# Kernel tuning notes

Measured on AMD Instinct MI355X. Metric: run time of the kernel, lower is better.

## Reference

```python
import jax, jax.numpy as jnp
import numpy as np
from itertools import combinations

A = 4          # anchor_points
K = 16         # neighbor_num
INTRA = A * (A - 1) // 2   # 6
CH = INTRA * 2 + A * A     # 28 = generator channels
B, N, S = 1, 8192, 4096
CIN, COUT = 64, 128


def cdist(x):
    # pairwise euclidean distances [B,N,N], zero-safe sqrt (zero grad at d=0)
    sq = jnp.sum(x * x, -1)
    d2 = sq[:, :, None] + sq[:, None, :] - 2.0 * jnp.einsum('bnc,bmc->bnm', x, x)
    d2 = jnp.maximum(d2, 0.0)
    m = d2 > 0
    return jnp.where(m, jnp.sqrt(jnp.where(m, d2, 1.0)), 0.0)


def index_points(points, idx):
    # points [B,N,...], idx [B,*] -> [B,*,...]
    return jax.vmap(lambda p, i: p[i])(points, idx)


def index_points_dists(dists, i1, i2):
    # dists [B,N,N]; result[b,...] = dists[b, i1[b,...], i2[b,...]]
    i1, i2 = jnp.broadcast_arrays(i1, i2)
    return jax.vmap(lambda d, a, b: d[a, b])(dists, i1, i2)


def generator(xyz):
    # RotationInvariantDistFea.forward(xyz, concat_raw_relative_fea=True)
    D = cdist(xyz)
    neg_nd, ni = jax.lax.top_k(-D, K)   # K >= A; smallest-K, sorted ascending
    nd = -neg_nd
    ai = ni[:, :, :A]
    # intra-anchor dists: dists to anchors 1..A-1 plus pairwise dists among them
    subs = [index_points_dists(D, ai[:, :, pi], ai[:, :, pj])[:, :, None]
            for pi, pj in combinations(range(1, A), 2)]
    intra = jnp.concatenate([nd[:, :, 1:A]] + subs, axis=2)  # [B,P,6]
    # inter-anchor dists: center anchors x neighbor anchors -> [B,P,K,A*A]
    nai = index_points(ai, ni)                                # [B,P,K,A]
    inter = index_points_dists(D, ai[:, :, None, :, None],
                               nai[:, :, :, None, :]).reshape(D.shape[0], D.shape[1], K, A * A)
    center = jnp.broadcast_to(intra[:, :, None, :], (intra.shape[0], intra.shape[1], K, INTRA))
    rf = jnp.concatenate([center, index_points(intra, ni), inter], axis=3)  # [B,P,K,28]
    return rf, ni, D


def mlp(x, W, b, g, be, act):
    # Linear + BatchNorm1d (training mode: stats over batch*points) + optional leaky_relu(0.2)
    y = x @ W + b
    mu = jnp.mean(y, (0, 1))
    var = jnp.var(y, (0, 1))
    y = (y - mu) * jax.lax.rsqrt(var + 1e-5) * g + be
    return jax.nn.leaky_relu(y, 0.2) if act else y


def forward(xyz, feature, sample_indexes, Ww, bw, gw, betaw, Wb, bb, gb, betab, Wo, bo, go, betao):
    rf_before, ni_before, D_before = generator(xyz)
    intra_before = rf_before[:, :, 0, :INTRA]
    xyz_s = index_points(xyz, sample_indexes)
    feat = index_points(feature, sample_indexes)
    intra_before = index_points(intra_before, sample_indexes)
    rf_after, ni_after, _ = generator(xyz_s)
    intra_after = rf_after[:, :, 0, :INTRA]
    a_before = index_points(ni_before[:, :, :A], sample_indexes)                  # [B,S,A]
    a_after = jax.vmap(lambda s, a: s[a])(sample_indexes, ni_after[:, :, :A])     # map to global idx
    inter = index_points_dists(D_before, a_before[:, :, :, None],
                               a_after[:, :, None, :]).reshape(B, S, A * A)
    adf = jnp.concatenate([intra_before, intra_after, inter], axis=2)             # [B,S,28]
    w = mlp(adf, Ww, bw, gw, betaw, False)
    bia = mlp(adf, Wb, bb, gb, betab, False)
    feat = jax.nn.leaky_relu(feat * w + bia, 0.2)
    feat = jnp.concatenate([feat, adf], axis=2)                                   # [B,S,92]
    feat = mlp(feat, Wo, bo, go, betao, True)                                     # [B,S,128]
    return xyz_s, feat, rf_after, ni_after


def setup_inputs():
    key = jax.random.key(0)
    ks = jax.random.split(key, 8)
    xyz = jax.random.normal(ks[0], (B, N, 3), jnp.float32)
    feature = jax.random.normal(ks[1], (B, N, CIN), jnp.float32)
    sample_indexes = jnp.stack([jax.random.permutation(jax.random.fold_in(ks[2], i), N)[:S]
                                for i in range(B)]).astype(jnp.int32)

    def lin(k, cin, cout):
        k1, k2 = jax.random.split(k)
        W = jax.random.normal(k1, (cin, cout), jnp.float32) / np.float32(np.sqrt(cin))
        b = jax.random.normal(k2, (cout,), jnp.float32) * 0.01
        return W, b, jnp.ones((cout,), jnp.float32), jnp.zeros((cout,), jnp.float32)

    Ww, bw, gw, betaw = lin(ks[5], CH, CIN)
    Wb, bb, gb, betab = lin(ks[6], CH, CIN)
    Wo, bo, go, betao = lin(ks[7], CH + CIN, COUT)
    return dict(xyz=xyz, feature=feature, sample_indexes=sample_indexes,
                Ww=Ww, bw=bw, gw=gw, betaw=betaw,
                Wb=Wb, bb=bb, gb=gb, betab=betab,
                Wo=Wo, bo=bo, go=go, betao=betao)


def reference(xyz, feature, sample_indexes, Ww, bw, gw, betaw, Wb, bb, gb, betab, Wo, bo, go, betao):
    return forward(xyz, feature, sample_indexes, Ww, bw, gw, betaw, Wb, bb, gb, betab, Wo, bo, go, betao)
```

## Files before the change

### kernel.cpp

```cpp
#include <hip/hip_runtime.h>
#include <hip/hip_bf16.h>
#include <math.h>

#define N_PTS 8192
#define S_PTS 4096
typedef unsigned long long u64;
typedef unsigned u32;

__device__ __forceinline__ float pair_dist_d(const float4 a, const float4 b) {
    double ax = a.x, ay = a.y, az = a.z;
    double bx = b.x, by = b.y, bz = b.z;
    double dx = ax - bx, dy = ay - by, dz = az - bz;
    double d2 = dx * dx + dy * dy + dz * dz;
    return d2 > 0.0 ? (float)sqrt(d2) : 0.0f;
}

__device__ __forceinline__ float d2_f32_gram(const float4 a, const float4 b) {
    float dot = __fadd_rn(__fadd_rn(__fmul_rn(a.x, b.x), __fmul_rn(a.y, b.y)),
                          __fmul_rn(a.z, b.z));
    float d2 = __fsub_rn(__fadd_rn(a.w, b.w), __fmul_rn(2.0f, dot));
    return fmaxf(d2, 0.0f);
}

__global__ __launch_bounds__(256) void stage_kernel(
        const float* __restrict__ xyz, const int* __restrict__ sidx,
        float4* __restrict__ cb, float4* __restrict__ ca,
        float* __restrict__ out_xyz_s) {
    int i = blockIdx.x * blockDim.x + threadIdx.x;
    if (i < N_PTS) {
        float x = xyz[i * 3 + 0], y = xyz[i * 3 + 1], z = xyz[i * 3 + 2];
        float sq = __fadd_rn(__fadd_rn(__fmul_rn(x, x), __fmul_rn(y, y)),
                             __fmul_rn(z, z));
        cb[i] = make_float4(x, y, z, sq);
    }
    if (i < S_PTS) {
        int si = sidx[i];
        float x = xyz[si * 3 + 0], y = xyz[si * 3 + 1], z = xyz[si * 3 + 2];
        float sq = __fadd_rn(__fadd_rn(__fmul_rn(x, x), __fmul_rn(y, y)),
                             __fmul_rn(z, z));
        ca[i] = make_float4(x, y, z, sq);
        out_xyz_s[i * 3 + 0] = x;
        out_xyz_s[i * 3 + 1] = y;
        out_xyz_s[i * 3 + 2] = z;
    }
}


template <int KOUT, int ITERS>
__device__ u64 knn_full_ladder(const float4 q, const float4* __restrict__ cand,
                               int lane) {
    u32 Lk[KOUT], Li[KOUT];
#pragma unroll
    for (int j = 0; j < KOUT; ++j) { Lk[j] = 0xFFFFFFFFu; Li[j] = 0xFFFFFFFFu; }
    int c = lane;
    for (int tt = 0; tt < ITERS; ++tt, c += 64) {
        float d2 = d2_f32_gram(q, cand[c]);
        float Df = d2 > 0.0f ? __fsqrt_rn(d2) : 0.0f;
        u32 kb = __float_as_uint(Df);
        if (kb < Lk[KOUT - 1]) {
#pragma unroll
            for (int j = KOUT - 1; j >= 1; --j) {
                bool up = kb < Lk[j - 1], ins = kb < Lk[j];
                Lk[j] = up ? Lk[j - 1] : (ins ? kb : Lk[j]);
                Li[j] = up ? Li[j - 1] : (ins ? (u32)c : Li[j]);
            }
            bool i0 = kb < Lk[0];
            Lk[0] = i0 ? kb : Lk[0];
            Li[0] = i0 ? (u32)c : Li[0];
        }
    }
    u64 Lu[KOUT];
#pragma unroll
    for (int j = 0; j < KOUT; ++j) Lu[j] = ((u64)Lk[j] << 32) | (u64)Li[j];
    u64 res = ~0ull;
#pragma unroll
    for (int r = 0; r < KOUT; ++r) {
        u64 m = Lu[0];
#pragma unroll
        for (int off = 32; off >= 1; off >>= 1) {
            u64 o = __shfl_xor(m, off, 64);
            m = (o < m) ? o : m;
        }
        if (lane == r) res = m;
        if (Lu[0] == m) {
#pragma unroll
            for (int j = 0; j < KOUT - 1; ++j) Lu[j] = Lu[j + 1];
            Lu[KOUT - 1] = ~0ull;
        }
    }
    return res;
}

template <int J, int K, int NC>
__device__ u64 knn_select(const float4 q, const float4* __restrict__ cand,
                          int t, u32* mins, u64* buf, u32* shm) {
    int lane = t & 63, wid = t >> 6;
    u32 d2b[J];
    u32 m = 0xFFFFFFFFu;
#pragma unroll
    for (int j = 0; j < J; ++j) {
        float d2 = d2_f32_gram(q, cand[t + 256 * j]);
        u32 b = __float_as_uint(d2);
        d2b[j] = b;
        m = b < m ? b : m;
    }
    mins[t] = m;
    __syncthreads();
    if (wid == 0) {
        u32 v = mins[lane];
        u32 v2 = mins[lane + 64];  v = v2 < v ? v2 : v;
        v2 = mins[lane + 128];     v = v2 < v ? v2 : v;
        v2 = mins[lane + 192];     v = v2 < v ? v2 : v;
#pragma unroll
        for (int k = 2; k <= 64; k <<= 1) {
#pragma unroll
            for (int j2 = k >> 1; j2 >= 1; j2 >>= 1) {
                u32 o = __shfl_xor(v, j2, 64);
                bool keepMin = (((lane & j2) == 0) == ((lane & k) == 0));
                bool less = o < v;
                v = keepMin ? (less ? o : v) : (less ? v : o);
            }
        }
        if (lane == K - 1) shm[0] = v;
    }
    __syncthreads();
    u32 tau = shm[0];
    u32 c = 0;
#pragma unroll
    for (int j = 0; j < J; ++j) c += (d2b[j] <= tau) ? 1u : 0u;
    u32 x = c;
#pragma unroll
    for (int off = 1; off < 64; off <<= 1) {
        u32 y = __shfl_up(x, off, 64);
        if (lane >= off) x += y;
    }
    if (lane == 63) shm[1 + wid] = x;
    __syncthreads();
    u32 base = x - c;
    for (int w = 0; w < wid; ++w) base += shm[1 + w];
    u32 cnt = shm[1] + shm[2] + shm[3] + shm[4];
    if (cnt <= 256u) {
        u32 off = base;
#pragma unroll
        for (int j = 0; j < J; ++j) {
            if (d2b[j] <= tau) {
                float d2 = __uint_as_float(d2b[j]);
                float D = d2 > 0.0f ? __fsqrt_rn(d2) : 0.0f;
                buf[off++] = ((u64)__float_as_uint(D) << 32) |
                             (u64)(u32)(t + 256 * j);
            }
        }
    }
    __syncthreads();
    u64 res = ~0ull;
    if (wid == 0) {
        if (cnt <= 64u) {
            u64 v = (lane < (int)cnt) ? buf[lane] : ~0ull;
#pragma unroll
            for (int k = 2; k <= 64; k <<= 1) {
#pragma unroll
                for (int j2 = k >> 1; j2 >= 1; j2 >>= 1) {
                    u64 o = __shfl_xor(v, j2, 64);
                    bool keepMin = (((lane & j2) == 0) == ((lane & k) == 0));
                    bool less = o < v;
                    v = keepMin ? (less ? o : v) : (less ? v : o);
                }
            }
            res = v;
        } else if (cnt <= 256u) {
            u64 L0 = ~0ull, L1 = ~0ull, L2 = ~0ull, L3 = ~0ull;
            for (u32 mm = lane; mm < cnt; mm += 64) {
                u64 kk = buf[mm];
                if (kk < L3) {
                    if (kk < L1) {
                        L3 = L2; L2 = L1;
                        if (kk < L0) { L1 = L0; L0 = kk; } else L1 = kk;
                    } else {
                        if (kk < L2) { L3 = L2; L2 = kk; } else L3 = kk;
                    }
                }
            }
#pragma unroll
            for (int r = 0; r < K; ++r) {
                u64 mr = L0;
#pragma unroll
                for (int off = 32; off >= 1; off >>= 1) {
                    u64 o = __shfl_xor(mr, off, 64);
                    mr = (o < mr) ? o : mr;
                }
                if (lane == r) res = mr;
                if (L0 == mr) { L0 = L1; L1 = L2; L2 = L3; L3 = ~0ull; }
            }
        } else {
            res = knn_full_ladder<K, NC / 64>(q, cand, lane);
        }
    }
    return res;
}

__global__ __launch_bounds__(256, 4) void knn_kernel(
        const float4* __restrict__ cb, const float4* __restrict__ ca,
        const int* __restrict__ sidx,
        int* __restrict__ a_before, float* __restrict__ intra_before,
        int* __restrict__ ni_i, float* __restrict__ intra_after,
        float* __restrict__ out_ni) {
    __shared__ u32 mins[256];
    __shared__ u64 buf[256];
    __shared__ u32 shm[8];
    int t = threadIdx.x, lane = t & 63, wid = t >> 6;
    int bid = blockIdx.x;
    if (bid < S_PTS) {
        int s = bid;
        float4 q = ca[s];
        u64 res = knn_select<16, 16, 4096>(q, ca, t, mins, buf, shm);
        if (wid == 0) {
            int idx = (int)(res & 0xffffffffull);
            if (lane < 16) {
                ni_i[s * 16 + lane] = idx;
                out_ni[s * 16 + lane] = (float)idx;
            }
            if (lane >= 1 && lane < 4)
                intra_after[s * 6 + (lane - 1)] = pair_dist_d(q, ca[idx]);
            int i1 = __shfl(idx, 1, 64);
            int i2 = __shfl(idx, 2, 64);
            int i3 = __shfl(idx, 3, 64);
            if (lane < 3) {
                int pa = (lane == 2) ? i2 : i1;
                int pb = (lane == 0) ? i2 : i3;
                intra_after[s * 6 + 3 + lane] = pair_dist_d(ca[pa], ca[pb]);
            }
        }
    } else {
        int s = bid - S_PTS;
        float4 q = cb[sidx[s]];
        u64 res = knn_select<32, 4, 8192>(q, cb, t, mins, buf, shm);
        if (wid == 0) {
            int idx = (int)(res & 0xffffffffull);
            if (lane < 4) a_before[s * 4 + lane] = idx;
            if (lane >= 1 && lane < 4)
                intra_before[s * 6 + (lane - 1)] = pair_dist_d(q, cb[idx]);
            int i1 = __shfl(idx, 1, 64);
            int i2 = __shfl(idx, 2, 64);
            int i3 = __shfl(idx, 3, 64);
            if (lane < 3) {
                int pa = (lane == 2) ? i2 : i1;
                int pb = (lane == 0) ? i2 : i3;
                intra_before[s * 6 + 3 + lane] = pair_dist_d(cb[pa], cb[pb]);
            }
        }
    }
}

__global__ __launch_bounds__(256) void assemble_kernel(
        const float4* __restrict__ ca, const float4* __restrict__ cb,
        const int* __restrict__ ni_i, const float* __restrict__ intra_after,
        const int* __restrict__ a_before, const float* __restrict__ intra_before,
        const int* __restrict__ sidx,
        float* __restrict__ out_rf, float* __restrict__ adf) {
    __shared__ int s_ni[4][16];
    __shared__ float s_rf[4][16 * 28];
    __shared__ float s_ia[4][8];
    int t = threadIdx.x, wid = t >> 6, lane = t & 63;
    int s = blockIdx.x * 4 + wid;
    if (lane < 16) s_ni[wid][lane] = ni_i[s * 16 + lane];
    if (lane < 6) s_ia[wid][lane] = intra_after[s * 6 + lane];
    __syncthreads();

    int k = lane >> 2, qq = lane & 3;
    int nai_q = ni_i[s_ni[wid][k] * 16 + qq];
    float4 pq = ca[nai_q];
#pragma unroll
    for (int p = 0; p < 4; ++p) {
        float4 pp = ca[s_ni[wid][p]];
        s_rf[wid][k * 28 + 12 + p * 4 + qq] = pair_dist_d(pp, pq);
    }
    for (int idx = lane; idx < 16 * 12; idx += 64) {
        int kk = idx / 12, c = idx % 12;
        float v = (c < 6) ? s_ia[wid][c] : intra_after[s_ni[wid][kk] * 6 + (c - 6)];
        s_rf[wid][kk * 28 + c] = v;
    }
    if (lane < 16) {
        int p = lane >> 2, q2 = lane & 3;
        int ib = a_before[s * 4 + p];
        int ia = sidx[s_ni[wid][q2]];
        adf[s * 28 + 12 + lane] = pair_dist_d(cb[ib], cb[ia]);
    } else if (lane >= 32 && lane < 38) {
        adf[s * 28 + (lane - 32)] = intra_before[s * 6 + (lane - 32)];
    } else if (lane >= 40 && lane < 46) {
        adf[s * 28 + 6 + (lane - 40)] = s_ia[wid][lane - 40];
    }
    __syncthreads();
    const int base = s * 16 * 28;
    for (int idx = lane; idx < 16 * 28; idx += 64) out_rf[base + idx] = s_rf[wid][idx];
}

__global__ __launch_bounds__(256) void mlp1_kernel(
        const float* __restrict__ adf,
        const float* __restrict__ Ww, const float* __restrict__ bw,
        const float* __restrict__ Wb, const float* __restrict__ bb,
        float* __restrict__ y_wb) {
    __shared__ float sW[28 * 128];
    __shared__ float sb[128];
    __shared__ float sA[32 * 28];
    int t = threadIdx.x;
    for (int i = t; i < 28 * 128; i += 256) {
        int k = i >> 7, c = i & 127;
        sW[i] = (c < 64) ? Ww[k * 64 + c] : Wb[k * 64 + (c - 64)];
    }
    if (t < 128) sb[t] = (t < 64) ? bw[t] : bb[t - 64];
    int s0 = blockIdx.x * 32;
    for (int i = t; i < 32 * 28; i += 256) sA[i] = adf[s0 * 28 + i];
    __syncthreads();
    int sl = t >> 3, grp = t & 7;
    int s = s0 + sl;
    float acc[16];
#pragma unroll
    for (int k = 0; k < 16; ++k) acc[k] = sb[grp * 16 + k];
    for (int k2 = 0; k2 < 28; ++k2) {
        float a = sA[sl * 28 + k2];
#pragma unroll
        for (int k = 0; k < 16; ++k)
            acc[k] = fmaf(a, sW[k2 * 128 + grp * 16 + k], acc[k]);
    }
#pragma unroll
    for (int k = 0; k < 16; ++k) y_wb[(grp * 16 + k) * 4096 + s] = acc[k];
}

__global__ __launch_bounds__(256) void stats_kernel(
        const float* __restrict__ y,
        const float* __restrict__ g0, const float* __restrict__ be0,
        const float* __restrict__ g1, const float* __restrict__ be1, int csplit,
        float* __restrict__ scale, float* __restrict__ shift) {
    int c = blockIdx.x;
    const float* p = y + c * 4096;
    float s1 = 0.0f, s2 = 0.0f;
    for (int i = threadIdx.x; i < 4096; i += 256) {
        float v = p[i];
        s1 += v;
        s2 = fmaf(v, v, s2);
    }
    __shared__ float l1[256], l2[256];
    l1[threadIdx.x] = s1;
    l2[threadIdx.x] = s2;
    __syncthreads();
    for (int off = 128; off; off >>= 1) {
        if (threadIdx.x < off) {
            l1[threadIdx.x] += l1[threadIdx.x + off];
            l2[threadIdx.x] += l2[threadIdx.x + off];
        }
        __syncthreads();
    }
    if (threadIdx.x == 0) {
        float mean = l1[0] * (1.0f / 4096.0f);
        float var = l2[0] * (1.0f / 4096.0f) - mean * mean;
        float g = (c < csplit) ? g0[c] : g1[c - csplit];
        float be = (c < csplit) ? be0[c] : be1[c - csplit];
        float sc = g / sqrtf(var + 1e-5f);
        scale[c] = sc;
        shift[c] = be - mean * sc;
    }
}

__global__ __launch_bounds__(256) void mlp2_kernel(
        const float* __restrict__ y_wb,
        const float* __restrict__ scale1, const float* __restrict__ shift1,
        const float* __restrict__ feature, const int* __restrict__ sidx,
        const float* __restrict__ adf,
        const float* __restrict__ Wo, const float* __restrict__ bo,
        float* __restrict__ y_o) {
    __shared__ float sW[92 * 128];
    __shared__ float t2[16 * 129];
    __shared__ float scat[16 * 92];
    int t = threadIdx.x;
    int s0 = blockIdx.x * 16;
    for (int i = t; i < 92 * 128; i += 256) sW[i] = Wo[i];
    for (int i = t; i < 16 * 128; i += 256) {
        int row = i & 15, c = i >> 4;
        t2[row * 129 + c] = fmaf(y_wb[c * 4096 + s0 + row], scale1[c], shift1[c]);
    }
    __syncthreads();
    for (int rr = 0; rr < 16; rr += 4) {
        int r = rr + (t >> 6);
        int c = t & 63;
        int si = sidx[s0 + r];
        float f = feature[si * 64 + c];
        float v = fmaf(f, t2[r * 129 + c], t2[r * 129 + 64 + c]);
        scat[r * 92 + c] = v >= 0.0f ? v : 0.2f * v;
    }
    for (int i = t; i < 16 * 28; i += 256) {
        int row = i / 28, k = i % 28;
        scat[row * 92 + 64 + k] = adf[(s0 + row) * 28 + k];
    }
    __syncthreads();
    int r = t >> 4, cg = t & 15;
    float acc[8];
#pragma unroll
    for (int j = 0; j < 8; ++j) acc[j] = bo[cg * 8 + j];
    for (int c = 0; c < 92; ++c) {
        float a = scat[r * 92 + c];
#pragma unroll
        for (int j = 0; j < 8; ++j)
            acc[j] = fmaf(a, sW[c * 128 + cg * 8 + j], acc[j]);
    }
    int s = s0 + r;
#pragma unroll
    for (int j = 0; j < 8; ++j) y_o[(cg * 8 + j) * 4096 + s] = acc[j];
}

__global__ __launch_bounds__(256) void final_kernel(
        const float* __restrict__ y_o,
        const float* __restrict__ scale, const float* __restrict__ shift,
        float* __restrict__ out_feat) {
    int tid = blockIdx.x * 256 + threadIdx.x;
    int j = tid >> 12;
    int s = tid & 4095;
    float v = fmaf(y_o[tid], scale[j], shift[j]);
    v = v >= 0.0f ? v : 0.2f * v;
    out_feat[s * 128 + j] = v;
}

extern "C" void kernel_launch(void* const* d_in, const int* in_sizes, int n_in,
                              void* d_out, int out_size, void* d_ws, size_t ws_size,
                              hipStream_t stream) {
    const float* xyz = (const float*)d_in[0];
    const float* feature = (const float*)d_in[1];
    const int* sidx = (const int*)d_in[2];
    const float* Ww = (const float*)d_in[3];
    const float* bw = (const float*)d_in[4];
    const float* gw = (const float*)d_in[5];
    const float* betaw = (const float*)d_in[6];
    const float* Wb = (const float*)d_in[7];
    const float* bb = (const float*)d_in[8];
    const float* gb = (const float*)d_in[9];
    const float* betab = (const float*)d_in[10];
    const float* Wo = (const float*)d_in[11];
    const float* bo = (const float*)d_in[12];
    const float* go = (const float*)d_in[13];
    const float* betao = (const float*)d_in[14];

    float* out = (float*)d_out;
    float* out_xyz = out;
    float* out_feat = out + 12288;
    float* out_rf = out + 12288 + 524288;
    float* out_ni = out + 12288 + 524288 + 1835008;

    float* ws = (float*)d_ws;
    float4* cb = (float4*)ws;
    float4* ca = (float4*)(ws + 32768);
    int* a_before = (int*)(ws + 49152);
    float* intra_before = ws + 65536;
    int* ni_i = (int*)(ws + 90112);
    float* intra_after = ws + 155648;
    float* adf = ws + 180224;
    float* y_wb = ws + 294912;
    float* y_o = ws + 819200;
    float* scale1 = ws + 1343488;
    float* shift1 = ws + 1343616;
    float* scale_o = ws + 1343744;
    float* shift_o = ws + 1343872;

    stage_kernel<<<32, 256, 0, stream>>>(xyz, sidx, cb, ca, out_xyz);
    knn_kernel<<<2 * S_PTS, 256, 0, stream>>>(cb, ca, sidx, a_before, intra_before,
                                              ni_i, intra_after, out_ni);
    assemble_kernel<<<1024, 256, 0, stream>>>(ca, cb, ni_i, intra_after, a_before,
                                              intra_before, sidx, out_rf, adf);
    mlp1_kernel<<<128, 256, 0, stream>>>(adf, Ww, bw, Wb, bb, y_wb);
    stats_kernel<<<128, 256, 0, stream>>>(y_wb, gw, betaw, gb, betab, 64, scale1, shift1);
    mlp2_kernel<<<256, 256, 0, stream>>>(y_wb, scale1, shift1, feature, sidx, adf, Wo, bo, y_o);
    stats_kernel<<<128, 256, 0, stream>>>(y_o, go, betao, go, betao, 128, scale_o, shift_o);
    final_kernel<<<2048, 256, 0, stream>>>(y_o, scale_o, shift_o, out_feat);
}
```

Measured before the change: 171.5 us.

## Batch 8 queries per block and fuse before/after kNN over shared candidate scan

```diff
diff --git a/kernel.cpp b/kernel.cpp
--- a/kernel.cpp
+++ b/kernel.cpp
@@ -4,6 +4,7 @@
 
 #define N_PTS 8192
 #define S_PTS 4096
+#define CAP 128
 typedef unsigned long long u64;
 typedef unsigned u32;
 
@@ -22,10 +23,38 @@
     return fmaxf(d2, 0.0f);
 }
 
+__device__ __forceinline__ u32 bitonic64_u32(u32 v, int lane) {
+#pragma unroll
+    for (int k = 2; k <= 64; k <<= 1) {
+#pragma unroll
+        for (int j2 = k >> 1; j2 >= 1; j2 >>= 1) {
+            u32 o = __shfl_xor(v, j2, 64);
+            bool keepMin = (((lane & j2) == 0) == ((lane & k) == 0));
+            bool less = o < v;
+            v = keepMin ? (less ? o : v) : (less ? v : o);
+        }
+    }
+    return v;
+}
+
+__device__ __forceinline__ u64 bitonic64_u64(u64 v, int lane) {
+#pragma unroll
+    for (int k = 2; k <= 64; k <<= 1) {
+#pragma unroll
+        for (int j2 = k >> 1; j2 >= 1; j2 >>= 1) {
+            u64 o = __shfl_xor(v, j2, 64);
+            bool keepMin = (((lane & j2) == 0) == ((lane & k) == 0));
+            bool less = o < v;
+            v = keepMin ? (less ? o : v) : (less ? v : o);
+        }
+    }
+    return v;
+}
+
 __global__ __launch_bounds__(256) void stage_kernel(
         const float* __restrict__ xyz, const int* __restrict__ sidx,
         float4* __restrict__ cb, float4* __restrict__ ca,
-        float* __restrict__ out_xyz_s) {
+        int* __restrict__ inv, float* __restrict__ out_xyz_s) {
     int i = blockIdx.x * blockDim.x + threadIdx.x;
     if (i < N_PTS) {
         float x = xyz[i * 3 + 0], y = xyz[i * 3 + 1], z = xyz[i * 3 + 2];
@@ -39,188 +68,196 @@
         float sq = __fadd_rn(__fadd_rn(__fmul_rn(x, x), __fmul_rn(y, y)),
                              __fmul_rn(z, z));
         ca[i] = make_float4(x, y, z, sq);
+        inv[si] = i;
         out_xyz_s[i * 3 + 0] = x;
         out_xyz_s[i * 3 + 1] = y;
         out_xyz_s[i * 3 + 2] = z;
     }
 }
 
-
-template <int KOUT, int ITERS>
-__device__ u64 knn_full_ladder(const float4 q, const float4* __restrict__ cand,
-                               int lane) {
-    u32 Lk[KOUT], Li[KOUT];
-#pragma unroll
-    for (int j = 0; j < KOUT; ++j) { Lk[j] = 0xFFFFFFFFu; Li[j] = 0xFFFFFFFFu; }
-    int c = lane;
-    for (int tt = 0; tt < ITERS; ++tt, c += 64) {
-        float d2 = d2_f32_gram(q, cand[c]);
-        float Df = d2 > 0.0f ? __fsqrt_rn(d2) : 0.0f;
-        u32 kb = __float_as_uint(Df);
-        if (kb < Lk[KOUT - 1]) {
-#pragma unroll
-            for (int j = KOUT - 1; j >= 1; --j) {
-                bool up = kb < Lk[j - 1], ins = kb < Lk[j];
-                Lk[j] = up ? Lk[j - 1] : (ins ? kb : Lk[j]);
-                Li[j] = up ? Li[j - 1] : (ins ? (u32)c : Li[j]);
-            }
-            bool i0 = kb < Lk[0];
-            Lk[0] = i0 ? kb : Lk[0];
-            Li[0] = i0 ? (u32)c : Li[0];
-        }
-    }
-    u64 Lu[KOUT];
-#pragma unroll
-    for (int j = 0; j < KOUT; ++j) Lu[j] = ((u64)Lk[j] << 32) | (u64)Li[j];
+template <int K, bool AFTER>
+__device__ u64 cold_ladder(const float4 q, const float4* __restrict__ cb,
+                           const int* __restrict__ inv, int lane) {
+    u64 L[K];
+#pragma unroll
+    for (int j = 0; j < K; ++j) L[j] = ~0ull;
+    for (int c = lane; c < N_PTS; c += 64) {
+        int low = c;
+        bool ok = true;
+        if (AFTER) { int iv = inv[c]; ok = iv >= 0; low = iv; }
+        if (!ok) continue;
+        float d2 = d2_f32_gram(q, cb[c]);
+        float D = d2 > 0.0f ? __fsqrt_rn(d2) : 0.0f;
+        u64 key = ((u64)__float_as_uint(D) << 32) | (u64)(u32)low;
+        if (key < L[K - 1]) {
+#pragma unroll
+            for (int j = K - 1; j >= 1; --j)
+                L[j] = (key < L[j - 1]) ? L[j - 1] : ((key < L[j]) ? key : L[j]);
+            L[0] = (key < L[0]) ? key : L[0];
+        }
+    }
     u64 res = ~0ull;
 #pragma unroll
-    for (int r = 0; r < KOUT; ++r) {
-        u64 m = Lu[0];
+    for (int r = 0; r < K; ++r) {
+        u64 m = L[0];
 #pragma unroll
         for (int off = 32; off >= 1; off >>= 1) {
             u64 o = __shfl_xor(m, off, 64);
             m = (o < m) ? o : m;
         }
         if (lane == r) res = m;
-        if (Lu[0] == m) {
-#pragma unroll
-            for (int j = 0; j < KOUT - 1; ++j) Lu[j] = Lu[j + 1];
-            Lu[KOUT - 1] = ~0ull;
+        if (L[0] == m) {
+#pragma unroll
+            for (int j = 0; j < K - 1; ++j) L[j] = L[j + 1];
+            L[K - 1] = ~0ull;
         }
     }
     return res;
 }
 
-template <int J, int K, int NC>
-__device__ u64 knn_select(const float4 q, const float4* __restrict__ cand,
-                          int t, u32* mins, u64* buf, u32* shm) {
-    int lane = t & 63, wid = t >> 6;
-    u32 d2b[J];
-    u32 m = 0xFFFFFFFFu;
-#pragma unroll
-    for (int j = 0; j < J; ++j) {
-        float d2 = d2_f32_gram(q, cand[t + 256 * j]);
-        u32 b = __float_as_uint(d2);
-        d2b[j] = b;
-        m = b < m ? b : m;
-    }
-    mins[t] = m;
-    __syncthreads();
-    if (wid == 0) {
-        u32 v = mins[lane];
-        u32 v2 = mins[lane + 64];  v = v2 < v ? v2 : v;
-        v2 = mins[lane + 128];     v = v2 < v ? v2 : v;
-        v2 = mins[lane + 192];     v = v2 < v ? v2 : v;
-#pragma unroll
-        for (int k = 2; k <= 64; k <<= 1) {
-#pragma unroll
-            for (int j2 = k >> 1; j2 >= 1; j2 >>= 1) {
-                u32 o = __shfl_xor(v, j2, 64);
-                bool keepMin = (((lane & j2) == 0) == ((lane & k) == 0));
-                bool less = o < v;
-                v = keepMin ? (less ? o : v) : (less ? v : o);
+template <int K>
+__device__ u64 finalize_sort(const u64* buf, u32 cnt, int lane) {
+    if (cnt <= 64u) {
+        u64 v = (lane < (int)cnt) ? buf[lane] : ~0ull;
+        return bitonic64_u64(v, lane);
+    }
+    u64 L0 = ~0ull, L1 = ~0ull, L2 = ~0ull, L3 = ~0ull;
+    for (u32 mm = lane; mm < cnt; mm += 64) {
+        u64 kk = buf[mm];
+        if (kk < L3) {
+            if (kk < L1) {
+                L3 = L2; L2 = L1;
+                if (kk < L0) { L1 = L0; L0 = kk; } else L1 = kk;
+            } else {
+                if (kk < L2) { L3 = L2; L2 = kk; } else L3 = kk;
             }
         }
-        if (lane == K - 1) shm[0] = v;
-    }
-    __syncthreads();
-    u32 tau = shm[0];
-    u32 c = 0;
-#pragma unroll
-    for (int j = 0; j < J; ++j) c += (d2b[j] <= tau) ? 1u : 0u;
-    u32 x = c;
-#pragma unroll
-    for (int off = 1; off < 64; off <<= 1) {
-        u32 y = __shfl_up(x, off, 64);
-        if (lane >= off) x += y;
-    }
-    if (lane == 63) shm[1 + wid] = x;
-    __syncthreads();
-    u32 base = x - c;
-    for (int w = 0; w < wid; ++w) base += shm[1 + w];
-    u32 cnt = shm[1] + shm[2] + shm[3] + shm[4];
-    if (cnt <= 256u) {
-        u32 off = base;
-#pragma unroll
-        for (int j = 0; j < J; ++j) {
-            if (d2b[j] <= tau) {
-                float d2 = __uint_as_float(d2b[j]);
-                float D = d2 > 0.0f ? __fsqrt_rn(d2) : 0.0f;
-                buf[off++] = ((u64)__float_as_uint(D) << 32) |
-                             (u64)(u32)(t + 256 * j);
-            }
-        }
-    }
-    __syncthreads();
+    }
     u64 res = ~0ull;
-    if (wid == 0) {
-        if (cnt <= 64u) {
-            u64 v = (lane < (int)cnt) ? buf[lane] : ~0ull;
-#pragma unroll
-            for (int k = 2; k <= 64; k <<= 1) {
-#pragma unroll
-                for (int j2 = k >> 1; j2 >= 1; j2 >>= 1) {
-                    u64 o = __shfl_xor(v, j2, 64);
-                    bool keepMin = (((lane & j2) == 0) == ((lane & k) == 0));
-                    bool less = o < v;
-                    v = keepMin ? (less ? o : v) : (less ? v : o);
-                }
-            }
-            res = v;
-        } else if (cnt <= 256u) {
-            u64 L0 = ~0ull, L1 = ~0ull, L2 = ~0ull, L3 = ~0ull;
-            for (u32 mm = lane; mm < cnt; mm += 64) {
-                u64 kk = buf[mm];
-                if (kk < L3) {
-                    if (kk < L1) {
-                        L3 = L2; L2 = L1;
-                        if (kk < L0) { L1 = L0; L0 = kk; } else L1 = kk;
-                    } else {
-                        if (kk < L2) { L3 = L2; L2 = kk; } else L3 = kk;
-                    }
-                }
-            }
-#pragma unroll
-            for (int r = 0; r < K; ++r) {
-                u64 mr = L0;
-#pragma unroll
-                for (int off = 32; off >= 1; off >>= 1) {
-                    u64 o = __shfl_xor(mr, off, 64);
-                    mr = (o < mr) ? o : mr;
-                }
-                if (lane == r) res = mr;
-                if (L0 == mr) { L0 = L1; L1 = L2; L2 = L3; L3 = ~0ull; }
-            }
-        } else {
-            res = knn_full_ladder<K, NC / 64>(q, cand, lane);
-        }
+#pragma unroll
+    for (int r = 0; r < K; ++r) {
+        u64 mr = L0;
+#pragma unroll
+        for (int off = 32; off >= 1; off >>= 1) {
+            u64 o = __shfl_xor(mr, off, 64);
+            mr = (o < mr) ? o : mr;
+        }
+        if (lane == r) res = mr;
+        if (L0 == mr) { L0 = L1; L1 = L2; L2 = L3; L3 = ~0ull; }
     }
     return res;
 }
 
-__global__ __launch_bounds__(256, 4) void knn_kernel(
+__global__ __launch_bounds__(256) void knn_kernel(
         const float4* __restrict__ cb, const float4* __restrict__ ca,
-        const int* __restrict__ sidx,
+        const int* __restrict__ inv, const int* __restrict__ sidx,
         int* __restrict__ a_before, float* __restrict__ intra_before,
         int* __restrict__ ni_i, float* __restrict__ intra_after,
         float* __restrict__ out_ni) {
-    __shared__ u32 mins[256];
-    __shared__ u64 buf[256];
-    __shared__ u32 shm[8];
+    __shared__ u32 smin[16][256];
+    __shared__ u64 sbuf[16][CAP];
+    __shared__ u32 staus[16];
+    __shared__ u32 scnt[16];
+    __shared__ float4 sq[8];
     int t = threadIdx.x, lane = t & 63, wid = t >> 6;
-    int bid = blockIdx.x;
-    if (bid < S_PTS) {
-        int s = bid;
-        float4 q = ca[s];
-        u64 res = knn_select<16, 16, 4096>(q, ca, t, mins, buf, shm);
-        if (wid == 0) {
+    int s0 = blockIdx.x * 8;
+    if (t < 8) sq[t] = cb[sidx[s0 + t]];
+    if (t < 16) scnt[t] = 0;
+    __syncthreads();
+    float4 q[8];
+#pragma unroll
+    for (int i = 0; i < 8; ++i) q[i] = sq[i];
+
+    u32 mB[8], mA[8];
+#pragma unroll
+    for (int i = 0; i < 8; ++i) { mB[i] = ~0u; mA[i] = ~0u; }
+    for (int c = t; c < N_PTS; c += 256) {
+        float4 p = cb[c];
+        bool smp = inv[c] >= 0;
+#pragma unroll
+        for (int i = 0; i < 8; ++i) {
+            u32 b = __float_as_uint(d2_f32_gram(q[i], p));
+            mB[i] = b < mB[i] ? b : mB[i];
+            if (smp) mA[i] = b < mA[i] ? b : mA[i];
+        }
+    }
+#pragma unroll
+    for (int i = 0; i < 8; ++i) { smin[i][t] = mB[i]; smin[8 + i][t] = mA[i]; }
+    __syncthreads();
+#pragma unroll
+    for (int m = 0; m < 4; ++m) {
+        int st = wid * 4 + m;
+        u32 v = smin[st][lane];
+        u32 v2 = smin[st][lane + 64];  v = v2 < v ? v2 : v;
+        v2 = smin[st][lane + 128];     v = v2 < v ? v2 : v;
+        v2 = smin[st][lane + 192];     v = v2 < v ? v2 : v;
+        v = bitonic64_u32(v, lane);
+        int kk = (st < 8) ? 3 : 15;
+        if (lane == kk) staus[st] = v;
+    }
+    __syncthreads();
+    u32 tB[8], tA[8];
+#pragma unroll
+    for (int i = 0; i < 8; ++i) { tB[i] = staus[i]; tA[i] = staus[8 + i]; }
+
+    for (int c = t; c < N_PTS; c += 256) {
+        float4 p = cb[c];
+        int iv = inv[c];
+        bool smp = iv >= 0;
+#pragma unroll
+        for (int i = 0; i < 8; ++i) {
+            u32 b = __float_as_uint(d2_f32_gram(q[i], p));
+            bool qb = b <= tB[i];
+            bool qa = smp && (b <= tA[i]);
+            if (qb || qa) {
+                float d2v = __uint_as_float(b);
+                float D = d2v > 0.0f ? __fsqrt_rn(d2v) : 0.0f;
+                u64 hk = (u64)__float_as_uint(D) << 32;
+                if (qb) {
+                    u32 pos = atomicAdd(&scnt[i], 1u);
+                    if (pos < CAP) sbuf[i][pos] = hk | (u64)(u32)c;
+                }
+                if (qa) {
+                    u32 pos = atomicAdd(&scnt[8 + i], 1u);
+                    if (pos < CAP) sbuf[8 + i][pos] = hk | (u64)(u32)iv;
+                }
+            }
+        }
+    }
+    __syncthreads();
+#pragma unroll
+    for (int m = 0; m < 4; ++m) {
+        int st = wid * 4 + m;
+        u32 cnt = scnt[st];
+        if (st < 8) {
+            int s = s0 + st;
+            float4 qq = q[st];
+            u64 res = (cnt <= CAP) ? finalize_sort<4>(sbuf[st], cnt, lane)
+                                   : cold_ladder<4, false>(qq, cb, inv, lane);
+            int idx = (int)(res & 0xffffffffull);
+            if (lane < 4) a_before[s * 4 + lane] = idx;
+            if (lane >= 1 && lane < 4)
+                intra_before[s * 6 + (lane - 1)] = pair_dist_d(qq, cb[idx]);
+            int i1 = __shfl(idx, 1, 64);
+            int i2 = __shfl(idx, 2, 64);
+            int i3 = __shfl(idx, 3, 64);
+            if (lane < 3) {
+                int pa = (lane == 2) ? i2 : i1;
+                int pb = (lane == 0) ? i2 : i3;
+                intra_before[s * 6 + 3 + lane] = pair_dist_d(cb[pa], cb[pb]);
+            }
+        } else {
+            int s = s0 + (st - 8);
+            float4 qq = q[st - 8];
+            u64 res = (cnt <= CAP) ? finalize_sort<16>(sbuf[st], cnt, lane)
+                                   : cold_ladder<16, true>(qq, cb, inv, lane);
             int idx = (int)(res & 0xffffffffull);
             if (lane < 16) {
                 ni_i[s * 16 + lane] = idx;
                 out_ni[s * 16 + lane] = (float)idx;
             }
             if (lane >= 1 && lane < 4)
-                intra_after[s * 6 + (lane - 1)] = pair_dist_d(q, ca[idx]);
+                intra_after[s * 6 + (lane - 1)] = pair_dist_d(qq, ca[idx]);
             int i1 = __shfl(idx, 1, 64);
             int i2 = __shfl(idx, 2, 64);
             int i3 = __shfl(idx, 3, 64);
@@ -228,24 +265,6 @@
                 int pa = (lane == 2) ? i2 : i1;
                 int pb = (lane == 0) ? i2 : i3;
                 intra_after[s * 6 + 3 + lane] = pair_dist_d(ca[pa], ca[pb]);
-            }
-        }
-    } else {
-        int s = bid - S_PTS;
-        float4 q = cb[sidx[s]];
-        u64 res = knn_select<32, 4, 8192>(q, cb, t, mins, buf, shm);
-        if (wid == 0) {
-            int idx = (int)(res & 0xffffffffull);
-            if (lane < 4) a_before[s * 4 + lane] = idx;
-            if (lane >= 1 && lane < 4)
-                intra_before[s * 6 + (lane - 1)] = pair_dist_d(q, cb[idx]);
-            int i1 = __shfl(idx, 1, 64);
-            int i2 = __shfl(idx, 2, 64);
-            int i3 = __shfl(idx, 3, 64);
-            if (lane < 3) {
-                int pa = (lane == 2) ? i2 : i1;
-                int pb = (lane == 0) ? i2 : i3;
-                intra_before[s * 6 + 3 + lane] = pair_dist_d(cb[pa], cb[pb]);
             }
         }
     }
@@ -458,10 +477,12 @@
     float* shift1 = ws + 1343616;
     float* scale_o = ws + 1343744;
     float* shift_o = ws + 1343872;
-
-    stage_kernel<<<32, 256, 0, stream>>>(xyz, sidx, cb, ca, out_xyz);
-    knn_kernel<<<2 * S_PTS, 256, 0, stream>>>(cb, ca, sidx, a_before, intra_before,
-                                              ni_i, intra_after, out_ni);
+    int* inv = (int*)(ws + 1344000);
+
+    hipMemsetAsync(inv, 0xFF, N_PTS * sizeof(int), stream);
+    stage_kernel<<<32, 256, 0, stream>>>(xyz, sidx, cb, ca, inv, out_xyz);
+    knn_kernel<<<512, 256, 0, stream>>>(cb, ca, inv, sidx, a_before, intra_before,
+                                        ni_i, intra_after, out_ni);
     assemble_kernel<<<1024, 256, 0, stream>>>(ca, cb, ni_i, intra_after, a_before,
                                               intra_before, sidx, out_rf, adf);
     mlp1_kernel<<<128, 256, 0, stream>>>(adf, Ww, bw, Wb, bb, y_wb);
```

New measurement: 189.6 us. 1.11x slower.
